# Kernel tuning notes

Measured on AMD Instinct MI355X. Metric: run time of the kernel, lower is better.

The kernel has to match this reference:

```python
import jax, jax.numpy as jnp
import numpy as np

LEN = 4096
DIM = 2048

def setup_inputs() -> dict:
    key = jax.random.key(0)
    ks = jax.random.split(key, 8)
    inv = 1.0 / np.sqrt(DIM)
    return {
        "x": jax.random.normal(ks[0], (LEN, DIM), dtype=jnp.float32),
        "Wk": jax.random.uniform(ks[1], (DIM, DIM), jnp.float32, -inv, inv),
        "Wr": jax.random.uniform(ks[2], (DIM, DIM), jnp.float32, -inv, inv),
        "Wv": jax.random.uniform(ks[3], (DIM, DIM), jnp.float32, -inv, inv),
        "mix_k": jax.random.uniform(ks[4], (DIM,), jnp.float32),
        "mix_r": jax.random.uniform(ks[5], (DIM,), jnp.float32),
        "last_x_mix_k": jax.random.normal(ks[6], (DIM,), dtype=jnp.float32),
        "last_x_mix_r": jax.random.normal(ks[7], (DIM,), dtype=jnp.float32),
    }

def _decay_mix(x, mix_param, last_x, fft_x, L):
    # sigmoid decay per channel, exponential progression mix^t  [L, D]
    mix = jax.nn.sigmoid(mix_param)
    t = jnp.arange(L)[:, None].astype(x.dtype)
    prog = jnp.power(mix[None, :], t)
    # causal conv of x with prog via FFT (zero-padded to 2L, keep first L)
    fft_prog = jnp.fft.rfft(prog, n=2 * L, axis=0)
    conv = jnp.fft.irfft(fft_x * fft_prog, n=2 * L, axis=0)[:L]
    return last_x * prog * mix + (1.0 - mix) * conv

def reference(x, Wk, Wr, Wv, mix_k, mix_r, last_x_mix_k, last_x_mix_r):
    L = x.shape[0]
    fft_x = jnp.fft.rfft(x, n=2 * L, axis=0)  # shared between k and r paths
    x_mix_k = _decay_mix(x, mix_k, last_x_mix_k, fft_x, L)
    x_mix_r = _decay_mix(x, mix_r, last_x_mix_r, fft_x, L)
    k = x_mix_k @ Wk.T
    r = x_mix_r @ Wr.T
    vk = jnp.square(jax.nn.relu(k)) @ Wv.T
    return jax.nn.sigmoid(r) * vk
```

## Files before the change

### kernel.cpp

```cpp
#include <hip/hip_runtime.h>
#include <hip/hip_bf16.h>
#include <math.h>

#define LEN 4096
#define DIM 2048

typedef __attribute__((ext_vector_type(8))) short s16x8;
typedef __attribute__((ext_vector_type(4))) float f32x4;

__device__ inline ushort f2bf(float f) {
  union { float f; unsigned u; } v; v.f = f;
  unsigned r = (v.u + 0x7FFFu + ((v.u >> 16) & 1u)) >> 16;
  return (ushort)r;
}

__device__ inline float bf2f(ushort b) {
  union { unsigned u; float f; } v; v.u = ((unsigned)b) << 16;
  return v.f;
}

__device__ inline void gll16(const void* g, void* l) {
  __builtin_amdgcn_global_load_lds(
      (const __attribute__((address_space(1))) void*)g,
      (__attribute__((address_space(3))) void*)l, 16, 0, 0);
}

__global__ __launch_bounds__(256) void wconv3(
    const float* __restrict__ Wk, const float* __restrict__ Wr,
    const float* __restrict__ Wv, ushort* __restrict__ Wkb,
    ushort* __restrict__ Wrb, ushort* __restrict__ Wvb) {
  int b = blockIdx.x;
  int which = b >> 12;
  int i = (b & 4095) * 1024 + threadIdx.x * 4;
  const float* W = which == 0 ? Wk : which == 1 ? Wr : Wv;
  ushort* O = which == 0 ? Wkb : which == 1 ? Wrb : Wvb;
  float4 v = *(const float4*)(W + i);
  ushort4 o;
  o.x = f2bf(v.x); o.y = f2bf(v.y); o.z = f2bf(v.z); o.w = f2bf(v.w);
  *(ushort4*)(O + i) = o;
}

#define CHUNK 64
#define WARM 64
__global__ __launch_bounds__(256) void ema_kernel(
    const float* __restrict__ x,
    const float* __restrict__ mix_k, const float* __restrict__ mix_r,
    const float* __restrict__ lastk, const float* __restrict__ lastr,
    ushort* __restrict__ xmk, ushort* __restrict__ xmr) {
  const int d = blockIdx.y * 256 + threadIdx.x;
  const int c = blockIdx.x;
  const float mk = 1.f / (1.f + expf(-mix_k[d]));
  const float mr = 1.f / (1.f + expf(-mix_r[d]));
  const float omk = 1.f - mk, omr = 1.f - mr;
  float ak, ar;
  const int t0 = c * CHUNK;
  if (c == 0) {
    ak = lastk[d]; ar = lastr[d];
  } else {
    ak = 0.f; ar = 0.f;
#pragma unroll 4
    for (int t = t0 - WARM; t < t0; ++t) {
      float xv = x[(size_t)t * DIM + d];
      ak = fmaf(mk, ak, omk * xv);
      ar = fmaf(mr, ar, omr * xv);
    }
  }
#pragma unroll 4
  for (int t = t0; t < t0 + CHUNK; ++t) {
    float xv = x[(size_t)t * DIM + d];
    ak = fmaf(mk, ak, omk * xv);
    ar = fmaf(mr, ar, omr * xv);
    xmk[(size_t)t * DIM + d] = f2bf(ak);
    xmr[(size_t)t * DIM + d] = f2bf(ar);
  }
}

#define BAR() __builtin_amdgcn_s_barrier()
#define LGKM0() asm volatile("s_waitcnt lgkmcnt(0)")
#define VM4() asm volatile("s_waitcnt vmcnt(4)" ::: "memory")

template <int EPI>
__device__ __forceinline__ void gemm8_body(
    const ushort* __restrict__ A, const ushort* __restrict__ B,
    float* __restrict__ Cf, ushort* __restrict__ Cb,
    const ushort* __restrict__ Sig, int bid, ushort* lds0, ushort* lds1) {
  const int N = DIM, K = DIM;
  const int tid = threadIdx.x;
  const int lane = tid & 63;
  const int w = tid >> 6;
  const int wr = w >> 2;
  const int wc = w & 3;
  const int tm = (bid >> 3) * 256;
  const int tn = (bid & 7) * 256;

  f32x4 acc[8][4];
#pragma unroll
  for (int i = 0; i < 8; ++i)
#pragma unroll
    for (int j = 0; j < 4; ++j)
      acc[i][j] = (f32x4){0.f, 0.f, 0.f, 0.f};

  const int sr = tid >> 3;
  const int ssw = ((tid & 7) ^ (sr & 7)) << 3;

  auto stA = [&](ushort* buf, int h, int kt) {
    ushort* dst = buf + h * 8192;
    int ke = kt * 64 + ssw;
    gll16(A + (size_t)(tm + h * 128 + sr) * K + ke, dst + tid * 8);
    gll16(A + (size_t)(tm + h * 128 + 64 + sr) * K + ke, dst + 4096 + tid * 8);
  };
  auto stB = [&](ushort* buf, int h, int kt) {
    ushort* dst = buf + 16384 + h * 8192;
    int ke = kt * 64 + ssw;
    gll16(B + (size_t)(tn + h * 128 + sr) * K + ke, dst + tid * 8);
    gll16(B + (size_t)(tn + h * 128 + 64 + sr) * K + ke, dst + 4096 + tid * 8);
  };

  s16x8 af[4][2], bf[4][2];
  auto rdA = [&](const ushort* buf, int qm) {
#pragma unroll
    for (int i = 0; i < 4; ++i)
#pragma unroll
      for (int kk = 0; kk < 2; ++kk) {
        int rr = (qm * 4 + i) * 16 + (lane & 15);
        int segp = ((kk << 2) + (lane >> 4)) ^ (lane & 7);
        af[i][kk] = *(const s16x8*)(buf + wr * 8192 + rr * 64 + segp * 8);
      }
  };
  auto rdB2 = [&](const ushort* buf, int qn) {
#pragma unroll
    for (int j = 0; j < 2; ++j)
#pragma unroll
      for (int kk = 0; kk < 2; ++kk) {
        int nn = wc * 64 + (qn * 2 + j) * 16 + (lane & 15);
        int segp = ((kk << 2) + (lane >> 4)) ^ (lane & 7);
        bf[qn * 2 + j][kk] =
            *(const s16x8*)(buf + 16384 + (nn >> 7) * 8192 + (nn & 127) * 64 + segp * 8);
      }
  };
  auto mm = [&](int qm, int qn) {
    __builtin_amdgcn_s_setprio(1);
#pragma unroll
    for (int i = 0; i < 4; ++i)
#pragma unroll
      for (int j = 0; j < 2; ++j)
#pragma unroll
        for (int kk = 0; kk < 2; ++kk)
          acc[qm * 4 + i][qn * 2 + j] = __builtin_amdgcn_mfma_f32_16x16x32_bf16(
              af[i][kk], bf[qn * 2 + j][kk], acc[qm * 4 + i][qn * 2 + j], 0, 0, 0);
    __builtin_amdgcn_s_setprio(0);
  };

  stA(lds0, 0, 0); stA(lds0, 1, 0); stB(lds0, 0, 0); stB(lds0, 1, 0);
  stB(lds1, 0, 1); stB(lds1, 1, 1);
  VM4();
  BAR();

  for (int u = 0; u < 16; ++u) {
    int k1 = 2 * u + 1;
    int k2 = 2 * u + 2 < 32 ? 2 * u + 2 : 31;
    int k3 = 2 * u + 3 < 32 ? 2 * u + 3 : 31;
    rdA(lds0, 0); rdB2(lds0, 0); stA(lds1, 0, k1);
    BAR(); LGKM0(); mm(0, 0); BAR();
    rdB2(lds0, 1); stA(lds1, 1, k1);
    BAR(); LGKM0(); mm(0, 1); BAR();
    rdA(lds0, 1); stB(lds0, 0, k2);
    BAR(); LGKM0(); mm(1, 0); BAR();
    stB(lds0, 1, k2); VM4();
    BAR(); mm(1, 1); BAR();
    rdA(lds1, 0); rdB2(lds1, 0); stA(lds0, 0, k2);
    BAR(); LGKM0(); mm(0, 0); BAR();
    rdB2(lds1, 1); stA(lds0, 1, k2);
    BAR(); LGKM0(); mm(0, 1); BAR();
    rdA(lds1, 1); stB(lds1, 0, k3);
    BAR(); LGKM0(); mm(1, 0); BAR();
    stB(lds1, 1, k3); VM4();
    BAR(); mm(1, 1); BAR();
  }

#pragma unroll
  for (int i = 0; i < 8; ++i)
#pragma unroll
    for (int j = 0; j < 4; ++j) {
      int col = tn + wc * 64 + j * 16 + (lane & 15);
#pragma unroll
      for (int q = 0; q < 4; ++q) {
        int row = tm + wr * 128 + i * 16 + (lane >> 4) * 4 + q;
        float v = acc[i][j][q];
        size_t o = (size_t)row * N + col;
        if (EPI == 0) {
          float rl = v > 0.f ? v : 0.f;
          Cb[o] = f2bf(rl * rl);
        } else if (EPI == 1) {
          Cb[o] = f2bf(1.f / (1.f + expf(-v)));
        } else {
          Cf[o] = bf2f(Sig[o]) * v;
        }
      }
    }
}

__global__ __launch_bounds__(512, 2) void gemm_kr(
    const ushort* __restrict__ Ak, const ushort* __restrict__ Bk,
    ushort* __restrict__ sq,
    const ushort* __restrict__ Ar, const ushort* __restrict__ Br,
    ushort* __restrict__ sig) {
  __shared__ __align__(16) ushort lds[2][32768];
  int lbid = (blockIdx.x & 7) * 32 + (blockIdx.x >> 3);
  if (lbid < 128)
    gemm8_body<0>(Ak, Bk, nullptr, sq, nullptr, lbid, lds[0], lds[1]);
  else
    gemm8_body<1>(Ar, Br, nullptr, sig, nullptr, lbid - 128, lds[0], lds[1]);
}

__global__ __launch_bounds__(512, 2) void gemm_v(
    const ushort* __restrict__ A, const ushort* __restrict__ B,
    float* __restrict__ Cf, const ushort* __restrict__ Sig) {
  __shared__ __align__(16) ushort lds[2][32768];
  int lbid = (blockIdx.x & 7) * 16 + (blockIdx.x >> 3);
  gemm8_body<2>(A, B, Cf, nullptr, Sig, lbid, lds[0], lds[1]);
}

extern "C" void kernel_launch(void* const* d_in, const int* in_sizes, int n_in,
                              void* d_out, int out_size, void* d_ws, size_t ws_size,
                              hipStream_t stream) {
  const float* x    = (const float*)d_in[0];
  const float* Wk   = (const float*)d_in[1];
  const float* Wr   = (const float*)d_in[2];
  const float* Wv   = (const float*)d_in[3];
  const float* mixk = (const float*)d_in[4];
  const float* mixr = (const float*)d_in[5];
  const float* lxk  = (const float*)d_in[6];
  const float* lxr  = (const float*)d_in[7];
  float* out = (float*)d_out;

  char* ws = (char*)d_ws;
  ushort* xmk = (ushort*)(ws);
  ushort* xmr = (ushort*)(ws + (16u << 20));
  ushort* Wkb = (ushort*)(ws + (32u << 20));
  ushort* Wrb = (ushort*)(ws + (40u << 20));
  ushort* Wvb = (ushort*)(ws + (48u << 20));
  ushort* sq  = (ushort*)(ws + (56u << 20));
  ushort* sig = (ushort*)(ws + (72u << 20));

  wconv3<<<3 * 4096, 256, 0, stream>>>(Wk, Wr, Wv, Wkb, Wrb, Wvb);

  ema_kernel<<<dim3(LEN / CHUNK, DIM / 256), 256, 0, stream>>>(
      x, mixk, mixr, lxk, lxr, xmk, xmr);

  gemm_kr<<<256, 512, 0, stream>>>(xmk, Wkb, sq, xmr, Wrb, sig);
  gemm_v<<<128, 512, 0, stream>>>(sq, Wvb, out, sig);
}
```

Baseline: 276.3 us.

## Merge prep kernels and retile gemm_v to 128x256 with triple-buffered LDS

The weight conversion and EMA kernels become one launch, with blocks split by index, to save a launch and let both kinds of work overlap. The final Wv GEMM switches from 256x256 tiles on 128 blocks to 128x256 tiles on 256 blocks. That fills all compute units on the 256-CU part, and a simpler loop with three LDS buffers prefetches two k-steps ahead. The smaller tiles reuse the B operand less, and LDS use per block rises to 144KB, which may limit occupancy.

```diff
diff --git a/kernel.cpp b/kernel.cpp
--- a/kernel.cpp
+++ b/kernel.cpp
@@ -25,65 +25,66 @@
       (__attribute__((address_space(3))) void*)l, 16, 0, 0);
 }
 
-__global__ __launch_bounds__(256) void wconv3(
+#define CHUNK 64
+#define WARM 64
+__global__ __launch_bounds__(256) void prep_kernel(
+    const float* __restrict__ x,
+    const float* __restrict__ mix_k, const float* __restrict__ mix_r,
+    const float* __restrict__ lastk, const float* __restrict__ lastr,
+    ushort* __restrict__ xmk, ushort* __restrict__ xmr,
     const float* __restrict__ Wk, const float* __restrict__ Wr,
     const float* __restrict__ Wv, ushort* __restrict__ Wkb,
     ushort* __restrict__ Wrb, ushort* __restrict__ Wvb) {
   int b = blockIdx.x;
-  int which = b >> 12;
-  int i = (b & 4095) * 1024 + threadIdx.x * 4;
-  const float* W = which == 0 ? Wk : which == 1 ? Wr : Wv;
-  ushort* O = which == 0 ? Wkb : which == 1 ? Wrb : Wvb;
-  float4 v = *(const float4*)(W + i);
-  ushort4 o;
-  o.x = f2bf(v.x); o.y = f2bf(v.y); o.z = f2bf(v.z); o.w = f2bf(v.w);
-  *(ushort4*)(O + i) = o;
-}
-
-#define CHUNK 64
-#define WARM 64
-__global__ __launch_bounds__(256) void ema_kernel(
-    const float* __restrict__ x,
-    const float* __restrict__ mix_k, const float* __restrict__ mix_r,
-    const float* __restrict__ lastk, const float* __restrict__ lastr,
-    ushort* __restrict__ xmk, ushort* __restrict__ xmr) {
-  const int d = blockIdx.y * 256 + threadIdx.x;
-  const int c = blockIdx.x;
-  const float mk = 1.f / (1.f + expf(-mix_k[d]));
-  const float mr = 1.f / (1.f + expf(-mix_r[d]));
-  const float omk = 1.f - mk, omr = 1.f - mr;
-  float ak, ar;
-  const int t0 = c * CHUNK;
-  if (c == 0) {
-    ak = lastk[d]; ar = lastr[d];
-  } else {
-    ak = 0.f; ar = 0.f;
+  if (b < 512) {
+    const int c = b & 63;
+    const int d = (b >> 6) * 256 + threadIdx.x;
+    const float mk = 1.f / (1.f + expf(-mix_k[d]));
+    const float mr = 1.f / (1.f + expf(-mix_r[d]));
+    const float omk = 1.f - mk, omr = 1.f - mr;
+    float ak, ar;
+    const int t0 = c * CHUNK;
+    if (c == 0) {
+      ak = lastk[d]; ar = lastr[d];
+    } else {
+      ak = 0.f; ar = 0.f;
 #pragma unroll 4
-    for (int t = t0 - WARM; t < t0; ++t) {
+      for (int t = t0 - WARM; t < t0; ++t) {
+        float xv = x[(size_t)t * DIM + d];
+        ak = fmaf(mk, ak, omk * xv);
+        ar = fmaf(mr, ar, omr * xv);
+      }
+    }
+#pragma unroll 4
+    for (int t = t0; t < t0 + CHUNK; ++t) {
       float xv = x[(size_t)t * DIM + d];
       ak = fmaf(mk, ak, omk * xv);
       ar = fmaf(mr, ar, omr * xv);
+      xmk[(size_t)t * DIM + d] = f2bf(ak);
+      xmr[(size_t)t * DIM + d] = f2bf(ar);
     }
-  }
-#pragma unroll 4
-  for (int t = t0; t < t0 + CHUNK; ++t) {
-    float xv = x[(size_t)t * DIM + d];
-    ak = fmaf(mk, ak, omk * xv);
-    ar = fmaf(mr, ar, omr * xv);
-    xmk[(size_t)t * DIM + d] = f2bf(ak);
-    xmr[(size_t)t * DIM + d] = f2bf(ar);
+  } else {
+    int wb = b - 512;
+    int which = wb >> 12;
+    int i = (wb & 4095) * 1024 + threadIdx.x * 4;
+    const float* W = which == 0 ? Wk : which == 1 ? Wr : Wv;
+    ushort* O = which == 0 ? Wkb : which == 1 ? Wrb : Wvb;
+    float4 v = *(const float4*)(W + i);
+    ushort4 o;
+    o.x = f2bf(v.x); o.y = f2bf(v.y); o.z = f2bf(v.z); o.w = f2bf(v.w);
+    *(ushort4*)(O + i) = o;
   }
 }
 
 #define BAR() __builtin_amdgcn_s_barrier()
 #define LGKM0() asm volatile("s_waitcnt lgkmcnt(0)")
 #define VM4() asm volatile("s_waitcnt vmcnt(4)" ::: "memory")
+#define VM6() asm volatile("s_waitcnt vmcnt(6)" ::: "memory")
 
 template <int EPI>
 __device__ __forceinline__ void gemm8_body(
     const ushort* __restrict__ A, const ushort* __restrict__ B,
-    float* __restrict__ Cf, ushort* __restrict__ Cb,
-    const ushort* __restrict__ Sig, int bid, ushort* lds0, ushort* lds1) {
+    ushort* __restrict__ Cb, int bid, ushort* lds0, ushort* lds1) {
   const int N = DIM, K = DIM;
   const int tid = threadIdx.x;
   const int lane = tid & 63;
@@ -191,10 +192,8 @@
         if (EPI == 0) {
           float rl = v > 0.f ? v : 0.f;
           Cb[o] = f2bf(rl * rl);
-        } else if (EPI == 1) {
+        } else {
           Cb[o] = f2bf(1.f / (1.f + expf(-v)));
-        } else {
-          Cf[o] = bf2f(Sig[o]) * v;
         }
       }
     }
@@ -208,17 +207,115 @@
   __shared__ __align__(16) ushort lds[2][32768];
   int lbid = (blockIdx.x & 7) * 32 + (blockIdx.x >> 3);
   if (lbid < 128)
-    gemm8_body<0>(Ak, Bk, nullptr, sq, nullptr, lbid, lds[0], lds[1]);
+    gemm8_body<0>(Ak, Bk, sq, lbid, lds[0], lds[1]);
   else
-    gemm8_body<1>(Ar, Br, nullptr, sig, nullptr, lbid - 128, lds[0], lds[1]);
+    gemm8_body<1>(Ar, Br, sig, lbid - 128, lds[0], lds[1]);
 }
 
 __global__ __launch_bounds__(512, 2) void gemm_v(
     const ushort* __restrict__ A, const ushort* __restrict__ B,
     float* __restrict__ Cf, const ushort* __restrict__ Sig) {
-  __shared__ __align__(16) ushort lds[2][32768];
-  int lbid = (blockIdx.x & 7) * 16 + (blockIdx.x >> 3);
-  gemm8_body<2>(A, B, Cf, nullptr, Sig, lbid, lds[0], lds[1]);
+  __shared__ __align__(16) ushort lds[3 * 24576];
+  const int N = DIM, K = DIM;
+  const int tid = threadIdx.x;
+  const int lane = tid & 63;
+  const int w = tid >> 6;
+  const int wr = w >> 2;
+  const int wc = w & 3;
+  int lbid = (blockIdx.x & 7) * 32 + (blockIdx.x >> 3);
+  const int tm = (lbid >> 3) * 128;
+  const int tn = (lbid & 7) * 256;
+
+  f32x4 acc[4][4];
+#pragma unroll
+  for (int i = 0; i < 4; ++i)
+#pragma unroll
+    for (int j = 0; j < 4; ++j)
+      acc[i][j] = (f32x4){0.f, 0.f, 0.f, 0.f};
+
+  const int sr = tid >> 3;
+  const int ssw = ((tid & 7) ^ (sr & 7)) << 3;
+
+  auto stA = [&](ushort* buf, int kt) {
+    int ke = kt * 64 + ssw;
+    gll16(A + (size_t)(tm + sr) * K + ke, buf + tid * 8);
+    gll16(A + (size_t)(tm + 64 + sr) * K + ke, buf + 4096 + tid * 8);
+  };
+  auto stB = [&](ushort* buf, int h, int kt) {
+    ushort* dst = buf + 8192 + h * 8192;
+    int ke = kt * 64 + ssw;
+    gll16(B + (size_t)(tn + h * 128 + sr) * K + ke, dst + tid * 8);
+    gll16(B + (size_t)(tn + h * 128 + 64 + sr) * K + ke, dst + 4096 + tid * 8);
+  };
+
+  s16x8 af[4][2], bf[4][2];
+  auto rdA = [&](const ushort* buf) {
+#pragma unroll
+    for (int i = 0; i < 4; ++i)
+#pragma unroll
+      for (int kk = 0; kk < 2; ++kk) {
+        int rr = wr * 64 + i * 16 + (lane & 15);
+        int segp = ((kk << 2) + (lane >> 4)) ^ (lane & 7);
+        af[i][kk] = *(const s16x8*)(buf + rr * 64 + segp * 8);
+      }
+  };
+  auto rdB = [&](const ushort* buf, int qn) {
+#pragma unroll
+    for (int j = 0; j < 2; ++j)
+#pragma unroll
+      for (int kk = 0; kk < 2; ++kk) {
+        int nn = wc * 64 + (qn * 2 + j) * 16 + (lane & 15);
+        int segp = ((kk << 2) + (lane >> 4)) ^ (lane & 7);
+        bf[qn * 2 + j][kk] =
+            *(const s16x8*)(buf + 8192 + (nn >> 7) * 8192 + (nn & 127) * 64 + segp * 8);
+      }
+  };
+  auto mm16 = [&](int qn) {
+    __builtin_amdgcn_s_setprio(1);
+#pragma unroll
+    for (int i = 0; i < 4; ++i)
+#pragma unroll
+      for (int j = 0; j < 2; ++j)
+#pragma unroll
+        for (int kk = 0; kk < 2; ++kk)
+          acc[i][qn * 2 + j] = __builtin_amdgcn_mfma_f32_16x16x32_bf16(
+              af[i][kk], bf[qn * 2 + j][kk], acc[i][qn * 2 + j], 0, 0, 0);
+    __builtin_amdgcn_s_setprio(0);
+  };
+
+  ushort* pc = lds;
+  ushort* pn = lds + 24576;
+  ushort* pn2 = lds + 49152;
+
+  stA(pc, 0); stB(pc, 0, 0); stB(pc, 1, 0);
+  stA(pn, 1); stB(pn, 0, 1); stB(pn, 1, 1);
+  VM6();
+  BAR();
+
+  for (int u = 0; u < 32; ++u) {
+    int kn = u + 2 < 32 ? u + 2 : 31;
+    rdA(pc); rdB(pc, 0);
+    stA(pn2, kn); stB(pn2, 0, kn);
+    BAR(); LGKM0(); mm16(0); BAR();
+    rdB(pc, 1);
+    stB(pn2, 1, kn);
+    VM6();
+    BAR(); LGKM0(); mm16(1); BAR();
+    ushort* t = pc; pc = pn; pn = pn2; pn2 = t;
+  }
+
+#pragma unroll
+  for (int i = 0; i < 4; ++i)
+#pragma unroll
+    for (int j = 0; j < 4; ++j) {
+      int col = tn + wc * 64 + j * 16 + (lane & 15);
+#pragma unroll
+      for (int q = 0; q < 4; ++q) {
+        int row = tm + wr * 64 + i * 16 + (lane >> 4) * 4 + q;
+        size_t o = (size_t)row * N + col;
+        Cf[o] = bf2f(Sig[o]) * acc[i][j][q];
+      }
+    }
 }
 
 extern "C" void kernel_launch(void* const* d_in, const int* in_sizes, int n_in,
@@ -243,11 +340,9 @@
   ushort* sq  = (ushort*)(ws + (56u << 20));
   ushort* sig = (ushort*)(ws + (72u << 20));
 
-  wconv3<<<3 * 4096, 256, 0, stream>>>(Wk, Wr, Wv, Wkb, Wrb, Wvb);
-
-  ema_kernel<<<dim3(LEN / CHUNK, DIM / 256), 256, 0, stream>>>(
-      x, mixk, mixr, lxk, lxr, xmk, xmr);
+  prep_kernel<<<512 + 3 * 4096, 256, 0, stream>>>(
+      x, mixk, mixr, lxk, lxr, xmk, xmr, Wk, Wr, Wv, Wkb, Wrb, Wvb);
 
   gemm_kr<<<256, 512, 0, stream>>>(xmk, Wkb, sq, xmr, Wrb, sig);
-  gemm_v<<<128, 512, 0, stream>>>(sq, Wvb, out, sig);
-}
+  gemm_v<<<256, 512, 0, stream>>>(sq, Wvb, out, sig);
+}
```

New measurement: 250.6 us. -9.3%, faster.
